# Kernel tuning notes

Measured on AMD Instinct MI355X. Metric: run time of the kernel, lower is better.

## Reference

```python
import math
import jax, jax.numpy as jnp
import numpy as np

B, S, D_MODEL, N_HEADS, D_KV = 1, 2048, 1024, 16, 64
NUM_BUCKETS, MAX_DIST = 32, 128


def _relative_position_bucket(rel_pos, bidirectional=True, num_buckets=32, max_distance=128):
    # rel_pos: int32 [S, S] = memory_pos - query_pos
    buckets = jnp.zeros_like(rel_pos)
    if bidirectional:
        num_buckets //= 2
        buckets = buckets + (rel_pos > 0).astype(jnp.int32) * num_buckets
        rel_pos = jnp.abs(rel_pos)
    else:
        rel_pos = -jnp.minimum(rel_pos, 0)
    max_exact = num_buckets // 2
    is_small = rel_pos < max_exact
    # log-spaced buckets for large distances; clamp arg to avoid log(0)
    rp_f = jnp.maximum(rel_pos, 1).astype(jnp.float32)
    large = max_exact + (
        jnp.log(rp_f / max_exact) / math.log(max_distance / max_exact) * (num_buckets - max_exact)
    ).astype(jnp.int32)
    large = jnp.minimum(large, num_buckets - 1)
    return buckets + jnp.where(is_small, rel_pos, large)


def setup_inputs() -> dict:
    key = jax.random.key(0)
    ks = jax.random.split(key, 6)
    scale = 1.0 / math.sqrt(D_MODEL)
    return {
        "hidden_states": jax.random.normal(ks[0], (B, S, D_MODEL), jnp.float32),
        "wq": jax.random.normal(ks[1], (D_MODEL, D_MODEL), jnp.float32) * scale,
        "wk": jax.random.normal(ks[2], (D_MODEL, D_MODEL), jnp.float32) * scale,
        "wv": jax.random.normal(ks[3], (D_MODEL, D_MODEL), jnp.float32) * scale,
        "wo": jax.random.normal(ks[4], (D_MODEL, D_MODEL), jnp.float32) * scale,
        "rel_bias": jax.random.normal(ks[5], (NUM_BUCKETS, N_HEADS), jnp.float32),
    }


def reference(hidden_states, wq, wk, wv, wo, rel_bias):
    b, s, _ = hidden_states.shape
    # projections (nn.Linear: x @ W.T), split heads -> [b, h, s, dk]
    def shape(x):
        return x.reshape(b, s, N_HEADS, D_KV).transpose(0, 2, 1, 3)

    q = shape(hidden_states @ wq.T)
    k = shape(hidden_states @ wk.T)
    v = shape(hidden_states @ wv.T)

    # T5: no 1/sqrt(d) scaling on scores
    scores = jnp.einsum("bhqd,bhkd->bhqk", q, k)

    # relative position bias: [1, h, s, s]
    rel_pos = jnp.arange(s, dtype=jnp.int32)[None, :] - jnp.arange(s, dtype=jnp.int32)[:, None]
    buckets = _relative_position_bucket(rel_pos, bidirectional=True,
                                        num_buckets=NUM_BUCKETS, max_distance=MAX_DIST)
    position_bias = rel_bias[buckets].transpose(2, 0, 1)[None]  # [1, h, s, s]

    attn = jax.nn.softmax(scores + position_bias, axis=-1)
    out = jnp.einsum("bhqk,bhkd->bhqd", attn, v)
    out = out.transpose(0, 2, 1, 3).reshape(b, s, N_HEADS * D_KV)
    return out @ wo.T
```

## Files before the change

kernel.cpp:

```cpp
#include <hip/hip_runtime.h>
#include <hip/hip_bf16.h>

typedef _Float16 f16;
typedef f16 f16x8 __attribute__((ext_vector_type(8)));
typedef f16 f16x4 __attribute__((ext_vector_type(4)));
typedef float f32x4 __attribute__((ext_vector_type(4)));

#define MFMA_F16(a, b, c) __builtin_amdgcn_mfma_f32_16x16x32_f16((a), (b), (c), 0, 0, 0)
#define LOG2E 1.44269504f

__device__ __forceinline__ void ld_lds16(const void* g, void* l) {
  __builtin_amdgcn_global_load_lds((const __attribute__((address_space(1))) void*)g,
                                   (__attribute__((address_space(3))) void*)l, 16, 0, 0);
}

__global__ __launch_bounds__(256) void cast_all(
    const float* __restrict__ hs, const float* __restrict__ wq,
    const float* __restrict__ wk, const float* __restrict__ wv,
    const float* __restrict__ wo, f16* __restrict__ hb,
    f16* __restrict__ wqb, f16* __restrict__ wkb,
    f16* __restrict__ wvb, f16* __restrict__ wob) {
  int idx = blockIdx.x * 256 + threadIdx.x;
  const float* src;
  f16* dst;
  int j;
  float scale = 1.0f;
  if (idx < 524288) {
    src = hs; dst = hb; j = idx;
  } else {
    int t = idx - 524288;
    int w = t >> 18;
    j = t & 262143;
    src = (w == 0) ? wq : (w == 1) ? wk : (w == 2) ? wv : wo;
    dst = (w == 0) ? wqb : (w == 1) ? wkb : (w == 2) ? wvb : wob;
    if (w == 0) scale = LOG2E;
  }
  float4 v = ((const float4*)src)[j];
  f16x4 o;
  o[0] = (f16)(v.x * scale); o[1] = (f16)(v.y * scale);
  o[2] = (f16)(v.z * scale); o[3] = (f16)(v.w * scale);
  ((f16x4*)dst)[j] = o;
}

__global__ __launch_bounds__(256) void build_bias(const float* __restrict__ rb,
                                                  float* __restrict__ btab) {
  int idx = blockIdx.x * 256 + threadIdx.x;
  int h = idx >> 12;
  int t = idx & 4095;
  int rel = t - 2047;
  int bucket = (rel > 0) ? 16 : 0;
  int a = (rel < 0) ? -rel : rel;
  int lg;
  if (a < 8) {
    lg = a;
  } else {
    int cnt = (a >= 12) + (a >= 16) + (a >= 23) + (a >= 32) + (a >= 46) +
              (a >= 64) + (a >= 91);
    lg = 8 + cnt;
  }
  bucket += lg;
  btab[idx] = rb[bucket * 16 + h] * LOG2E;
}

__device__ __forceinline__ void gemm_mainloop(const f16* __restrict__ A,
                                              const f16* __restrict__ B,
                                              int brow, int bcol,
                                              f16 (*lA)[64 * 64],
                                              f16 (*lB)[128 * 64],
                                              f32x4 acc[4][2]) {
  const int tid = threadIdx.x;
  const int lane = tid & 63;
  const int wn = tid >> 6;
  const int lo = lane & 15;
  const int hi = lane >> 4;
  const int sw = lo & 7;
  const int sr = tid >> 3;
  const int se = (((tid & 7) ^ (sr & 7)) << 3);
  const f16* gA = A + (size_t)(brow + sr) * 1024 + se;
  const f16* gB = B + (size_t)(bcol + sr) * 1024 + se;

#define GSTAGE(bi, k0_)                                                        \
  do {                                                                         \
    ld_lds16(gA + (k0_),             lA[bi] + tid * 8);                        \
    ld_lds16(gA + (k0_) + 32 * 1024, lA[bi] + tid * 8 + 2048);                 \
    ld_lds16(gB + (k0_),             lB[bi] + tid * 8);                        \
    ld_lds16(gB + (k0_) + 32 * 1024, lB[bi] + tid * 8 + 2048);                 \
    ld_lds16(gB + (k0_) + 64 * 1024, lB[bi] + tid * 8 + 4096);                 \
    ld_lds16(gB + (k0_) + 96 * 1024, lB[bi] + tid * 8 + 6144);                 \
  } while (0)

  GSTAGE(0, 0);
  __syncthreads();
  for (int k0 = 0; k0 < 1024; k0 += 64) {
    const int bi = (k0 >> 6) & 1;
    if (k0 < 960) GSTAGE(bi ^ 1, k0 + 64);
    f16x8 af[4][2], bf[2][2];
#pragma unroll
    for (int m = 0; m < 4; ++m)
#pragma unroll
      for (int ks = 0; ks < 2; ++ks)
        af[m][ks] = *(const f16x8*)(lA[bi] + (m * 16 + lo) * 64 +
                                    (((ks << 2) | hi) ^ sw) * 8);
#pragma unroll
    for (int j = 0; j < 2; ++j)
#pragma unroll
      for (int ks = 0; ks < 2; ++ks)
        bf[j][ks] = *(const f16x8*)(lB[bi] + (wn * 32 + j * 16 + lo) * 64 +
                                    (((ks << 2) | hi) ^ sw) * 8);
    __builtin_amdgcn_s_setprio(1);
#pragma unroll
    for (int m = 0; m < 4; ++m)
#pragma unroll
      for (int j = 0; j < 2; ++j)
#pragma unroll
        for (int ks = 0; ks < 2; ++ks)
          acc[m][j] = MFMA_F16(af[m][ks], bf[j][ks], acc[m][j]);
    __builtin_amdgcn_s_setprio(0);
    __syncthreads();
  }
#undef GSTAGE
}

__global__ __launch_bounds__(256) void gemm_qkv(
    const f16* __restrict__ A, const f16* __restrict__ Wq,
    const f16* __restrict__ Wk, const f16* __restrict__ Wv,
    f16* __restrict__ Qo, f16* __restrict__ Ko, f16* __restrict__ VTo) {
  __shared__ __align__(16) f16 lA[2][64 * 64];
  __shared__ __align__(16) f16 lB[2][128 * 64];
  const int z = blockIdx.z;
  const f16* B = (z == 0) ? Wq : (z == 1) ? Wk : Wv;
  const int brow = blockIdx.x * 64, bcol = blockIdx.y * 128;
  f32x4 acc[4][2];
#pragma unroll
  for (int m = 0; m < 4; ++m)
#pragma unroll
    for (int j = 0; j < 2; ++j) acc[m][j] = f32x4{0.f, 0.f, 0.f, 0.f};
  gemm_mainloop(A, B, brow, bcol, lA, lB, acc);
  const int lane = threadIdx.x & 63, wn = threadIdx.x >> 6;
  const int lo = lane & 15, hi = lane >> 4;
  if (z < 2) {
    f16* C = z ? Ko : Qo;
#pragma unroll
    for (int m = 0; m < 4; ++m)
#pragma unroll
      for (int j = 0; j < 2; ++j) {
        int col = bcol + wn * 32 + j * 16 + lo;
        int row0 = brow + m * 16 + hi * 4;
#pragma unroll
        for (int r = 0; r < 4; ++r)
          C[(size_t)(row0 + r) * 1024 + col] = (f16)acc[m][j][r];
      }
  } else {
#pragma unroll
    for (int m = 0; m < 4; ++m)
#pragma unroll
      for (int j = 0; j < 2; ++j) {
        int col = bcol + wn * 32 + j * 16 + lo;
        int g = m * 4 + hi;
        int w = g & 7;
        int gp = (g & 8) | ((w < 4) ? (2 * w) : (2 * (w - 4) + 1));
        int sp = brow + gp * 4;
        f16x4 v4;
#pragma unroll
        for (int r = 0; r < 4; ++r) v4[r] = (f16)acc[m][j][r];
        *(f16x4*)(VTo + (size_t)col * 2048 + sp) = v4;
      }
  }
}

__global__ __launch_bounds__(256) void gemm_out(const f16* __restrict__ A,
                                                const f16* __restrict__ W,
                                                float* __restrict__ C) {
  __shared__ __align__(16) f16 lA[2][64 * 64];
  __shared__ __align__(16) f16 lB[2][128 * 64];
  const int brow = blockIdx.x * 64, bcol = blockIdx.y * 128;
  f32x4 acc[4][2];
#pragma unroll
  for (int m = 0; m < 4; ++m)
#pragma unroll
    for (int j = 0; j < 2; ++j) acc[m][j] = f32x4{0.f, 0.f, 0.f, 0.f};
  gemm_mainloop(A, W, brow, bcol, lA, lB, acc);
  const int lane = threadIdx.x & 63, wn = threadIdx.x >> 6;
  const int lo = lane & 15, hi = lane >> 4;
#pragma unroll
  for (int m = 0; m < 4; ++m)
#pragma unroll
    for (int j = 0; j < 2; ++j) {
      int col = bcol + wn * 32 + j * 16 + lo;
      int row0 = brow + m * 16 + hi * 4;
#pragma unroll
      for (int r = 0; r < 4; ++r)
        C[(size_t)(row0 + r) * 1024 + col] = acc[m][j][r];
    }
}

__global__ __launch_bounds__(256, 2) void attn_kernel(
    const f16* __restrict__ Q, const f16* __restrict__ K,
    const f16* __restrict__ VT, const float* __restrict__ btab,
    f16* __restrict__ AO) {
  __shared__ __align__(16) f16 lK[2][4096];
  __shared__ __align__(16) f16 lV[2][4096];

  const int h = blockIdx.y;
  const int q0 = blockIdx.x * 64;
  const int tid = threadIdx.x;
  const int wave = tid >> 6, lane = tid & 63;
  const int lo = lane & 15, hi = lane >> 4;
  const int sw = lo & 7;
  const int qlo = q0 + wave * 16;
  const int myq = qlo + lo;

  const f16* Kh = K + h * 64;
  const f16* VTh = VT + (size_t)h * 64 * 2048;
  const float* bt = btab + h * 4096 + 2047 - myq;

  f16x8 qf[2];
#pragma unroll
  for (int kk = 0; kk < 2; ++kk)
    qf[kk] = *(const f16x8*)(Q + (size_t)myq * 1024 + h * 64 + kk * 32 + hi * 8);

  const float bp = btab[h * 4096 + 4094];
  const float bn = btab[h * 4096 + 0];

  const int sc0 = wave * 64 + lane;
  const int sc1 = 256 + sc0;
  const int r0 = sc0 >> 3, e0 = (sc0 & 7) ^ (r0 & 7);
  const int r1 = sc1 >> 3, e1 = (sc1 & 7) ^ (r1 & 7);

#define STAGE(bufi, kv)                                                        \
  do {                                                                         \
    ld_lds16(Kh + (size_t)((kv) + r0) * 1024 + e0 * 8, &lK[bufi][sc0 * 8]);    \
    ld_lds16(Kh + (size_t)((kv) + r1) * 1024 + e1 * 8, &lK[bufi][sc1 * 8]);    \
    ld_lds16(VTh + (size_t)r0 * 2048 + (kv) + e0 * 8, &lV[bufi][sc0 * 8]);     \
    ld_lds16(VTh + (size_t)r1 * 2048 + (kv) + e1 * 8, &lV[bufi][sc1 * 8]);     \
  } while (0)

  float m_run = -1e30f, l_run = 0.f;
  f32x4 oacc[4];
#pragma unroll
  for (int d = 0; d < 4; ++d) oacc[d] = f32x4{0.f, 0.f, 0.f, 0.f};

  f16x8 vfA[4][2], vfB[4][2];
  f32x4 saccA[4], saccB[4];
  float biasA[16], biasB[16];

#define TILE_FRONT(t_, CUR)                                                    \
  {                                                                            \
    const int b_ = (t_) & 1;                                                   \
    const int kv0_ = (t_) * 64;                                                \
    const f16* lKb_ = lK[b_];                                                  \
    const f16* lVb_ = lV[b_];                                                  \
    f16x8 kf_[4][2];                                                           \
    _Pragma("unroll") for (int m_ = 0; m_ < 4; ++m_)                           \
      _Pragma("unroll") for (int kk_ = 0; kk_ < 2; ++kk_)                      \
        kf_[m_][kk_] = *(const f16x8*)&lKb_[(m_ * 16 + lo) * 64 +              \
                                            (((kk_ << 2) | hi) ^ sw) * 8];     \
    _Pragma("unroll") for (int d_ = 0; d_ < 4; ++d_)                           \
      _Pragma("unroll") for (int kk_ = 0; kk_ < 2; ++kk_)                      \
        vf##CUR[d_][kk_] = *(const f16x8*)&lVb_[(d_ * 16 + lo) * 64 +          \
                                                ((kk_ * 4 + hi) ^ sw) * 8];    \
    if ((t_) < 31) STAGE(1 - b_, kv0_ + 64);                                   \
    {                                                                          \
      const int rmin_ = kv0_ - (qlo + 15);                                     \
      const int rmax_ = kv0_ + 63 - qlo;                                       \
      if (rmin_ >= 91 || rmax_ <= -91) {                                       \
        const float bf_ = (rmin_ >= 91) ? bp : bn;                             \
        _Pragma("unroll") for (int i_ = 0; i_ < 16; ++i_) bias##CUR[i_] = bf_; \
      } else {                                                                 \
        _Pragma("unroll") for (int i_ = 0; i_ < 16; ++i_)                      \
          bias##CUR[i_] = bt[kv0_ + (i_ >> 2) * 16 + hi * 4 + (i_ & 3)];       \
      }                                                                        \
    }                                                                          \
    __builtin_amdgcn_s_setprio(1);                                             \
    _Pragma("unroll") for (int m_ = 0; m_ < 4; ++m_) {                         \
      sacc##CUR[m_] = f32x4{0.f, 0.f, 0.f, 0.f};                               \
      _Pragma("unroll") for (int kk_ = 0; kk_ < 2; ++kk_)                      \
        sacc##CUR[m_] = MFMA_F16(kf_[m_][kk_], qf[kk_], sacc##CUR[m_]);        \
    }                                                                          \
    __builtin_amdgcn_s_setprio(0);                                             \
  }

#define SOFTMAX_PV(PRV)                                                        \
  {                                                                            \
    float p_[16];                                                              \
    float mx_ = -1e30f;                                                        \
    _Pragma("unroll") for (int i_ = 0; i_ < 16; ++i_) {                        \
      float s_ = sacc##PRV[i_ >> 2][i_ & 3] + bias##PRV[i_];                   \
      p_[i_] = s_;                                                             \
      mx_ = fmaxf(mx_, s_);                                                    \
    }                                                                          \
    mx_ = fmaxf(mx_, __shfl_xor(mx_, 16, 64));                                 \
    mx_ = fmaxf(mx_, __shfl_xor(mx_, 32, 64));                                 \
    if (!__all(mx_ <= m_run + 11.5416f)) {                                     \
      float mn_ = fmaxf(m_run, mx_);                                           \
      float sc_ = exp2f(m_run - mn_);                                          \
      l_run *= sc_;                                                            \
      _Pragma("unroll") for (int d_ = 0; d_ < 4; ++d_) oacc[d_] *= sc_;        \
      m_run = mn_;                                                             \
    }                                                                          \
    float ps_ = 0.f;                                                           \
    _Pragma("unroll") for (int i_ = 0; i_ < 16; ++i_) {                        \
      p_[i_] = exp2f(p_[i_] - m_run);                                          \
      ps_ += p_[i_];                                                           \
    }                                                                          \
    ps_ += __shfl_xor(ps_, 16, 64);                                            \
    ps_ += __shfl_xor(ps_, 32, 64);                                            \
    l_run += ps_;                                                              \
    f16x8 pf_[2];                                                              \
    _Pragma("unroll") for (int kk_ = 0; kk_ < 2; ++kk_)                        \
      _Pragma("unroll") for (int j_ = 0; j_ < 8; ++j_)                         \
        pf_[kk_][j_] = (f16)p_[(kk_ * 2 + (j_ >> 2)) * 4 + (j_ & 3)];          \
    __builtin_amdgcn_s_setprio(1);                                             \
    _Pragma("unroll") for (int d_ = 0; d_ < 4; ++d_)                           \
      _Pragma("unroll") for (int kk_ = 0; kk_ < 2; ++kk_)                      \
        oacc[d_] = MFMA_F16(vf##PRV[d_][kk_], pf_[kk_], oacc[d_]);             \
    __builtin_amdgcn_s_setprio(0);                                             \
  }

  STAGE(0, 0);
  __syncthreads();

  TILE_FRONT(0, A);
  __syncthreads();

  for (int k2 = 0; k2 < 15; ++k2) {
    const int t1 = 2 * k2 + 1;
    TILE_FRONT(t1, B);
    SOFTMAX_PV(A);
    __syncthreads();
    TILE_FRONT(t1 + 1, A);
    SOFTMAX_PV(B);
    __syncthreads();
  }
  TILE_FRONT(31, B);
  SOFTMAX_PV(A);
  SOFTMAX_PV(B);

#undef TILE_FRONT
#undef SOFTMAX_PV
#undef STAGE

  float inv = 1.f / l_run;
#pragma unroll
  for (int d = 0; d < 4; ++d) {
    f16x4 ov;
#pragma unroll
    for (int r = 0; r < 4; ++r) ov[r] = (f16)(oacc[d][r] * inv);
    *(f16x4*)(AO + (size_t)myq * 1024 + h * 64 + d * 16 + hi * 4) = ov;
  }
}

extern "C" void kernel_launch(void* const* d_in, const int* in_sizes, int n_in,
                              void* d_out, int out_size, void* d_ws, size_t ws_size,
                              hipStream_t stream) {
  const float* hs = (const float*)d_in[0];
  const float* wq = (const float*)d_in[1];
  const float* wk = (const float*)d_in[2];
  const float* wv = (const float*)d_in[3];
  const float* wo = (const float*)d_in[4];
  const float* rb = (const float*)d_in[5];

  char* w = (char*)d_ws;
  f16* hb  = (f16*)w; w += (size_t)2048 * 1024 * 2;
  f16* wqb = (f16*)w; w += (size_t)1024 * 1024 * 2;
  f16* wkb = (f16*)w; w += (size_t)1024 * 1024 * 2;
  f16* wvb = (f16*)w; w += (size_t)1024 * 1024 * 2;
  f16* wob = (f16*)w; w += (size_t)1024 * 1024 * 2;
  f16* Qb  = (f16*)w; w += (size_t)2048 * 1024 * 2;
  f16* Kb  = (f16*)w; w += (size_t)2048 * 1024 * 2;
  f16* VTb = (f16*)w; w += (size_t)2048 * 1024 * 2;
  f16* AOb = (f16*)w; w += (size_t)2048 * 1024 * 2;
  float* btab = (float*)w; w += (size_t)16 * 4096 * 4;

  cast_all<<<6144, 256, 0, stream>>>(hs, wq, wk, wv, wo, hb, wqb, wkb, wvb, wob);
  build_bias<<<256, 256, 0, stream>>>(rb, btab);
  gemm_qkv<<<dim3(32, 8, 3), 256, 0, stream>>>(hb, wqb, wkb, wvb, Qb, Kb, VTb);
  attn_kernel<<<dim3(32, 16), 256, 0, stream>>>(Qb, Kb, VTb, btab, AOb);
  gemm_out<<<dim3(32, 8), 256, 0, stream>>>(AOb, wob, (float*)d_out);
}
```

Measured before the change: 93.83 us.

## Prefetch bias one tile ahead, seed QK accumulators with bias, shrink out-GEMM tile

The attention kernel now loads the relative-position bias for the next KV tile while the current one is processed. It feeds the bias in as the initial MFMA accumulator, which removes the separate add in softmax. The row max and row sum reductions become trees to shorten dependency chains. Separately, the output GEMM is templated to a 32-row tile and launched on twice as many blocks to fill more CUs, at the cost of less reuse of the weight tile.

```diff
diff --git a/kernel.cpp b/kernel.cpp
--- a/kernel.cpp
+++ b/kernel.cpp
@@ -62,12 +62,13 @@
   btab[idx] = rb[bucket * 16 + h] * LOG2E;
 }
 
+template <int MR>
 __device__ __forceinline__ void gemm_mainloop(const f16* __restrict__ A,
                                               const f16* __restrict__ B,
                                               int brow, int bcol,
-                                              f16 (*lA)[64 * 64],
+                                              f16 (*lA)[MR * 16 * 64],
                                               f16 (*lB)[128 * 64],
-                                              f32x4 acc[4][2]) {
+                                              f32x4 acc[MR][2]) {
   const int tid = threadIdx.x;
   const int lane = tid & 63;
   const int wn = tid >> 6;
@@ -81,8 +82,9 @@
 
 #define GSTAGE(bi, k0_)                                                        \
   do {                                                                         \
-    ld_lds16(gA + (k0_),             lA[bi] + tid * 8);                        \
-    ld_lds16(gA + (k0_) + 32 * 1024, lA[bi] + tid * 8 + 2048);                 \
+    ld_lds16(gA + (k0_), lA[bi] + tid * 8);                                    \
+    if constexpr (MR == 4)                                                     \
+      ld_lds16(gA + (k0_) + 32 * 1024, lA[bi] + tid * 8 + 2048);               \
     ld_lds16(gB + (k0_),             lB[bi] + tid * 8);                        \
     ld_lds16(gB + (k0_) + 32 * 1024, lB[bi] + tid * 8 + 2048);                 \
     ld_lds16(gB + (k0_) + 64 * 1024, lB[bi] + tid * 8 + 4096);                 \
@@ -94,9 +96,9 @@
   for (int k0 = 0; k0 < 1024; k0 += 64) {
     const int bi = (k0 >> 6) & 1;
     if (k0 < 960) GSTAGE(bi ^ 1, k0 + 64);
-    f16x8 af[4][2], bf[2][2];
-#pragma unroll
-    for (int m = 0; m < 4; ++m)
+    f16x8 af[MR][2], bf[2][2];
+#pragma unroll
+    for (int m = 0; m < MR; ++m)
 #pragma unroll
       for (int ks = 0; ks < 2; ++ks)
         af[m][ks] = *(const f16x8*)(lA[bi] + (m * 16 + lo) * 64 +
@@ -109,7 +111,7 @@
                                     (((ks << 2) | hi) ^ sw) * 8);
     __builtin_amdgcn_s_setprio(1);
 #pragma unroll
-    for (int m = 0; m < 4; ++m)
+    for (int m = 0; m < MR; ++m)
 #pragma unroll
       for (int j = 0; j < 2; ++j)
 #pragma unroll
@@ -135,7 +137,7 @@
   for (int m = 0; m < 4; ++m)
 #pragma unroll
     for (int j = 0; j < 2; ++j) acc[m][j] = f32x4{0.f, 0.f, 0.f, 0.f};
-  gemm_mainloop(A, B, brow, bcol, lA, lB, acc);
+  gemm_mainloop<4>(A, B, brow, bcol, lA, lB, acc);
   const int lane = threadIdx.x & 63, wn = threadIdx.x >> 6;
   const int lo = lane & 15, hi = lane >> 4;
   if (z < 2) {
@@ -171,19 +173,19 @@
 __global__ __launch_bounds__(256) void gemm_out(const f16* __restrict__ A,
                                                 const f16* __restrict__ W,
                                                 float* __restrict__ C) {
-  __shared__ __align__(16) f16 lA[2][64 * 64];
+  __shared__ __align__(16) f16 lA[2][32 * 64];
   __shared__ __align__(16) f16 lB[2][128 * 64];
-  const int brow = blockIdx.x * 64, bcol = blockIdx.y * 128;
-  f32x4 acc[4][2];
-#pragma unroll
-  for (int m = 0; m < 4; ++m)
+  const int brow = blockIdx.x * 32, bcol = blockIdx.y * 128;
+  f32x4 acc[2][2];
+#pragma unroll
+  for (int m = 0; m < 2; ++m)
 #pragma unroll
     for (int j = 0; j < 2; ++j) acc[m][j] = f32x4{0.f, 0.f, 0.f, 0.f};
-  gemm_mainloop(A, W, brow, bcol, lA, lB, acc);
+  gemm_mainloop<2>(A, W, brow, bcol, lA, lB, acc);
   const int lane = threadIdx.x & 63, wn = threadIdx.x >> 6;
   const int lo = lane & 15, hi = lane >> 4;
 #pragma unroll
-  for (int m = 0; m < 4; ++m)
+  for (int m = 0; m < 2; ++m)
 #pragma unroll
     for (int j = 0; j < 2; ++j) {
       int col = bcol + wn * 32 + j * 16 + lo;
@@ -235,6 +237,20 @@
     ld_lds16(VTh + (size_t)r1 * 2048 + (kv) + e1 * 8, &lV[bufi][sc1 * 8]);     \
   } while (0)
 
+#define BIAS_LOAD(t_, ST)                                                      \
+  {                                                                            \
+    const int kb_ = (t_) * 64;                                                 \
+    const int rmin_ = kb_ - (qlo + 15);                                        \
+    const int rmax_ = kb_ + 63 - qlo;                                          \
+    if (rmin_ >= 91 || rmax_ <= -91) {                                         \
+      const float bf_ = (rmin_ >= 91) ? bp : bn;                               \
+      _Pragma("unroll") for (int i_ = 0; i_ < 16; ++i_) bias##ST[i_] = bf_;    \
+    } else {                                                                   \
+      _Pragma("unroll") for (int i_ = 0; i_ < 16; ++i_)                        \
+        bias##ST[i_] = bt[kb_ + (i_ >> 2) * 16 + hi * 4 + (i_ & 3)];           \
+    }                                                                          \
+  }
+
   float m_run = -1e30f, l_run = 0.f;
   f32x4 oacc[4];
 #pragma unroll
@@ -244,10 +260,9 @@
   f32x4 saccA[4], saccB[4];
   float biasA[16], biasB[16];
 
-#define TILE_FRONT(t_, CUR)                                                    \
+#define TILE_FRONT(t_, CUR, NXT)                                               \
   {                                                                            \
     const int b_ = (t_) & 1;                                                   \
-    const int kv0_ = (t_) * 64;                                                \
     const f16* lKb_ = lK[b_];                                                  \
     const f16* lVb_ = lV[b_];                                                  \
     f16x8 kf_[4][2];                                                           \
@@ -259,21 +274,12 @@
       _Pragma("unroll") for (int kk_ = 0; kk_ < 2; ++kk_)                      \
         vf##CUR[d_][kk_] = *(const f16x8*)&lVb_[(d_ * 16 + lo) * 64 +          \
                                                 ((kk_ * 4 + hi) ^ sw) * 8];    \
-    if ((t_) < 31) STAGE(1 - b_, kv0_ + 64);                                   \
-    {                                                                          \
-      const int rmin_ = kv0_ - (qlo + 15);                                     \
-      const int rmax_ = kv0_ + 63 - qlo;                                       \
-      if (rmin_ >= 91 || rmax_ <= -91) {                                       \
-        const float bf_ = (rmin_ >= 91) ? bp : bn;                             \
-        _Pragma("unroll") for (int i_ = 0; i_ < 16; ++i_) bias##CUR[i_] = bf_; \
-      } else {                                                                 \
-        _Pragma("unroll") for (int i_ = 0; i_ < 16; ++i_)                      \
-          bias##CUR[i_] = bt[kv0_ + (i_ >> 2) * 16 + hi * 4 + (i_ & 3)];       \
-      }                                                                        \
-    }                                                                          \
+    if ((t_) < 31) STAGE(1 - b_, (t_) * 64 + 64);                              \
+    if ((t_) < 31) BIAS_LOAD((t_) + 1, NXT);                                   \
     __builtin_amdgcn_s_setprio(1);                                             \
     _Pragma("unroll") for (int m_ = 0; m_ < 4; ++m_) {                         \
-      sacc##CUR[m_] = f32x4{0.f, 0.f, 0.f, 0.f};                               \
+      sacc##CUR[m_] = f32x4{bias##CUR[m_ * 4 + 0], bias##CUR[m_ * 4 + 1],      \
+                            bias##CUR[m_ * 4 + 2], bias##CUR[m_ * 4 + 3]};     \
       _Pragma("unroll") for (int kk_ = 0; kk_ < 2; ++kk_)                      \
         sacc##CUR[m_] = MFMA_F16(kf_[m_][kk_], qf[kk_], sacc##CUR[m_]);        \
     }                                                                          \
@@ -283,12 +289,15 @@
 #define SOFTMAX_PV(PRV)                                                        \
   {                                                                            \
     float p_[16];                                                              \
-    float mx_ = -1e30f;                                                        \
-    _Pragma("unroll") for (int i_ = 0; i_ < 16; ++i_) {                        \
-      float s_ = sacc##PRV[i_ >> 2][i_ & 3] + bias##PRV[i_];                   \
-      p_[i_] = s_;                                                             \
-      mx_ = fmaxf(mx_, s_);                                                    \
-    }                                                                          \
+    _Pragma("unroll") for (int i_ = 0; i_ < 16; ++i_)                          \
+      p_[i_] = sacc##PRV[i_ >> 2][i_ & 3];                                     \
+    float x8_[8];                                                              \
+    _Pragma("unroll") for (int i_ = 0; i_ < 8; ++i_)                           \
+      x8_[i_] = fmaxf(p_[i_], p_[i_ + 8]);                                     \
+    float x4_[4];                                                              \
+    _Pragma("unroll") for (int i_ = 0; i_ < 4; ++i_)                           \
+      x4_[i_] = fmaxf(x8_[i_], x8_[i_ + 4]);                                   \
+    float mx_ = fmaxf(fmaxf(x4_[0], x4_[1]), fmaxf(x4_[2], x4_[3]));           \
     mx_ = fmaxf(mx_, __shfl_xor(mx_, 16, 64));                                 \
     mx_ = fmaxf(mx_, __shfl_xor(mx_, 32, 64));                                 \
     if (!__all(mx_ <= m_run + 11.5416f)) {                                     \
@@ -298,11 +307,15 @@
       _Pragma("unroll") for (int d_ = 0; d_ < 4; ++d_) oacc[d_] *= sc_;        \
       m_run = mn_;                                                             \
     }                                                                          \
-    float ps_ = 0.f;                                                           \
-    _Pragma("unroll") for (int i_ = 0; i_ < 16; ++i_) {                        \
+    _Pragma("unroll") for (int i_ = 0; i_ < 16; ++i_)                          \
       p_[i_] = exp2f(p_[i_] - m_run);                                          \
-      ps_ += p_[i_];                                                           \
-    }                                                                          \
+    float s8_[8];                                                              \
+    _Pragma("unroll") for (int i_ = 0; i_ < 8; ++i_)                           \
+      s8_[i_] = p_[i_] + p_[i_ + 8];                                           \
+    float s4_[4];                                                              \
+    _Pragma("unroll") for (int i_ = 0; i_ < 4; ++i_)                           \
+      s4_[i_] = s8_[i_] + s8_[i_ + 4];                                         \
+    float ps_ = (s4_[0] + s4_[1]) + (s4_[2] + s4_[3]);                         \
     ps_ += __shfl_xor(ps_, 16, 64);                                            \
     ps_ += __shfl_xor(ps_, 32, 64);                                            \
     l_run += ps_;                                                              \
@@ -317,27 +330,29 @@
     __builtin_amdgcn_s_setprio(0);                                             \
   }
 
+  BIAS_LOAD(0, A);
   STAGE(0, 0);
   __syncthreads();
 
-  TILE_FRONT(0, A);
+  TILE_FRONT(0, A, B);
   __syncthreads();
 
   for (int k2 = 0; k2 < 15; ++k2) {
     const int t1 = 2 * k2 + 1;
-    TILE_FRONT(t1, B);
+    TILE_FRONT(t1, B, A);
     SOFTMAX_PV(A);
     __syncthreads();
-    TILE_FRONT(t1 + 1, A);
+    TILE_FRONT(t1 + 1, A, B);
     SOFTMAX_PV(B);
     __syncthreads();
   }
-  TILE_FRONT(31, B);
+  TILE_FRONT(31, B, A);
   SOFTMAX_PV(A);
   SOFTMAX_PV(B);
 
 #undef TILE_FRONT
 #undef SOFTMAX_PV
+#undef BIAS_LOAD
 #undef STAGE
 
   float inv = 1.f / l_run;
@@ -376,5 +391,5 @@
   build_bias<<<256, 256, 0, stream>>>(rb, btab);
   gemm_qkv<<<dim3(32, 8, 3), 256, 0, stream>>>(hb, wqb, wkb, wvb, Qb, Kb, VTb);
   attn_kernel<<<dim3(32, 16), 256, 0, stream>>>(Qb, Kb, VTb, btab, AOb);
-  gemm_out<<<dim3(32, 8), 256, 0, stream>>>(AOb, wob, (float*)d_out);
-}
+  gemm_out<<<dim3(64, 8), 256, 0, stream>>>(AOb, wob, (float*)d_out);
+}
```

Result: faster. 91.73 us, median of 2 (-2.2%).
